# Kernel optimization log

Hardware: AMD Instinct MI355X
Metric: run time of the kernel (lower is better)

Reference implementation:

```python
import jax, jax.numpy as jnp
import numpy as np
from jax import lax

N, L, B = 256, 20, 10      # batch, max_seq (baskets), max_bas (items/basket)
D, H, ASP, K = 128, 128, 4, 16  # dim, h, aspects, nbNUM
NITEMS = 20000
H2 = 2 * H


def setup_inputs() -> dict:
    key = jax.random.key(0)
    ks = jax.random.split(key, 20)
    nrm = lambda k, shape, s=0.05: (jax.random.normal(k, shape) * s).astype(jnp.float32)
    seq = jax.random.randint(ks[0], (N, L, B), 0, NITEMS + 1)          # indices into itemEmb
    uHis = jax.random.uniform(ks[1], (N, NITEMS), dtype=jnp.float32)   # dense user history
    itemEmb = nrm(ks[2], (NITEMS + 1, D), 0.1).at[0].set(0.0)          # padding_idx=0 row zeroed
    fc1_w = nrm(ks[3], (1, L * B * D)); fc1_b = jnp.zeros((1,), jnp.float32)
    aspProju = nrm(ks[4], (ASP, 1, H))
    aspProji = nrm(ks[5], (ASP, D, H))
    dh_w = nrm(ks[6], (H, D)); dh_b = jnp.zeros((H,), jnp.float32)
    wih0 = nrm(ks[7], (4 * H2, H2)); whh0 = nrm(ks[8], (4 * H2, H2))
    bih0 = jnp.zeros((4 * H2,), jnp.float32); bhh0 = jnp.zeros((4 * H2,), jnp.float32)
    wih1 = nrm(ks[9], (4 * H2, H2)); whh1 = nrm(ks[10], (4 * H2, H2))
    bih1 = jnp.zeros((4 * H2,), jnp.float32); bhh1 = jnp.zeros((4 * H2,), jnp.float32)
    out_w = nrm(ks[11], (NITEMS, H2)); out_b = jnp.zeros((NITEMS,), jnp.float32)
    his_w = nrm(ks[12], (H2, NITEMS)); his_b = jnp.zeros((H2,), jnp.float32)
    g1_w = nrm(ks[13], (1, H2)); g1_b = jnp.zeros((1,), jnp.float32)
    g2_w = nrm(ks[14], (1, H2)); g2_b = jnp.zeros((1,), jnp.float32)
    return dict(seq=seq, uHis=uHis, itemEmb=itemEmb, fc1_w=fc1_w, fc1_b=fc1_b,
                aspProju=aspProju, aspProji=aspProji, dh_w=dh_w, dh_b=dh_b,
                wih0=wih0, whh0=whh0, bih0=bih0, bhh0=bhh0,
                wih1=wih1, whh1=whh1, bih1=bih1, bhh1=bhh1,
                out_w=out_w, out_b=out_b, his_w=his_w, his_b=his_b,
                g1_w=g1_w, g1_b=g1_b, g2_w=g2_w, g2_b=g2_b)


def _lstm_layer(x, wih, whh, bih, bhh):
    # x: [N, T, in]; PyTorch gate order i, f, g, o
    Hs = whh.shape[1]
    def step(carry, xt):
        h, c = carry
        g = xt @ wih.T + bih + h @ whh.T + bhh
        i, f, gg, o = jnp.split(g, 4, axis=-1)
        c = jax.nn.sigmoid(f) * c + jax.nn.sigmoid(i) * jnp.tanh(gg)
        h = jax.nn.sigmoid(o) * jnp.tanh(c)
        return (h, c), h
    h0 = jnp.zeros((x.shape[0], Hs), x.dtype)
    _, ys = lax.scan(step, (h0, h0), jnp.swapaxes(x, 0, 1))
    return jnp.swapaxes(ys, 0, 1)


def reference(seq, uHis, itemEmb, fc1_w, fc1_b, aspProju, aspProji, dh_w, dh_b,
              wih0, whh0, bih0, bhh0, wih1, whh1, bih1, bhh1,
              out_w, out_b, his_w, his_b, g1_w, g1_b, g2_w, g2_b):
    n, l, b = seq.shape
    embs = itemEmb[seq]                                   # [N,L,B,D]
    # MIE_user: fresh fc1 -> scalar per user, project per aspect
    u_embs = embs.reshape(n, -1) @ fc1_w.T + fc1_b        # [N,1]
    userAsp = jnp.tanh(jnp.einsum('no,aoh->nah', u_embs, aspProju))      # [N,ASP,H]
    # MIE_item
    itemAsp = jnp.tanh(jnp.einsum('nlbd,adh->nalbh', embs, aspProji))    # [N,ASP,L,B,H]
    # SNA: per-aspect exact L2 kNN over the batch (FAISS IndexFlatL2 equivalent)
    uA = jnp.transpose(jnp.tanh(userAsp), (1, 0, 2))      # [ASP,N,H] (double tanh, as in source)
    sq = jnp.sum(uA * uA, -1)                             # [ASP,N]
    dist = sq[:, :, None] + sq[:, None, :] - 2.0 * jnp.einsum('anh,amh->anm', uA, uA)
    dist = jnp.where(jnp.eye(n, dtype=bool)[None], -1.0, dist)   # self ranked first
    _, I = lax.top_k(lax.stop_gradient(-dist), K)         # [ASP,N,K] ascending distance
    I = I[:, :, 1:]                                       # drop self -> K-1 neighbors
    # sum of neighbor embeddings via multiplicity matmul (== gather+sum)
    M = jax.nn.one_hot(I, n, dtype=embs.dtype).sum(2)     # [ASP,N,N]
    nb_sum = jnp.einsum('apn,nlbd->aplbd', M, embs)       # [ASP,N,L,B,D]
    nb_h = nb_sum @ dh_w.T + dh_b                         # [ASP,N,L,B,H]
    embs_PI = jnp.transpose(nb_h.sum(axis=3), (1, 0, 2, 3))        # [N,ASP,L,H]
    embs_UI = jnp.tanh(itemAsp).sum(axis=3)               # [N,ASP,L,H] (double tanh)
    neighbAsps = jnp.concatenate([embs_UI, embs_PI], axis=-1)      # [N,ASP,L,2H]
    # raw view (not permute!) then max-pool over last dim of size ASP
    x = jnp.reshape(neighbAsps, (n, l, H2, ASP)).max(axis=-1)      # [N,L,2H]
    # 2-layer LSTM (eval mode: inter-layer dropout inactive)
    y = _lstm_layer(x, wih0, whh0, bih0, bhh0)
    y = _lstm_layer(y, wih1, whh1, bih1, bhh1)
    h_agg = jnp.tanh(y.sum(axis=1))                       # [N,2H]
    probs = jax.nn.softmax(h_agg @ out_w.T + out_b, axis=-1)       # [N,NITEMS]
    uHis_h = uHis @ his_w.T + his_b                        # [N,2H]
    gate = jax.nn.sigmoid(uHis_h @ g1_w.T + g1_b + h_agg @ g2_w.T + g2_b)  # [N,1]
    scores = gate * probs + (1.0 - gate) * uHis
    return scores
```

## Files before the change

kernel.cpp:

```cpp
#include <hip/hip_runtime.h>
#include <math.h>

#define N_ 256
#define L_ 20
#define B_ 10
#define D_ 128
#define H_ 128
#define ASP_ 4
#define KK_ 16
#define NIT_ 20000
#define H2_ 256
#define G4_ 1024
#define LBD_ 25600
#define NL_ 5120
#define NLB_ 51200

typedef __attribute__((ext_vector_type(8))) short bf16x8;
typedef __attribute__((ext_vector_type(4))) short bf16x4;
typedef __attribute__((ext_vector_type(4))) float f32x4;

__device__ __forceinline__ float sigf(float x){ return 1.0f/(1.0f+expf(-x)); }
__device__ __forceinline__ float sigf_fast(float x){
  return __builtin_amdgcn_rcpf(1.0f + __expf(-x));
}
__device__ __forceinline__ float tanh_fast(float x){
  return 1.0f - 2.0f*__builtin_amdgcn_rcpf(__expf(2.0f*x) + 1.0f);
}
__device__ __forceinline__ unsigned short f2b(float f){
  unsigned int u = __float_as_uint(f);
  unsigned int r = (u + 0x7FFFu + ((u>>16)&1u)) >> 16;
  return (unsigned short)r;
}
__device__ __forceinline__ float b2f(unsigned short b){
  return __uint_as_float(((unsigned int)b) << 16);
}

__global__ void k_gather(const int* __restrict__ seq, const float* __restrict__ itemEmb,
                         float* __restrict__ embs, unsigned short* __restrict__ ebh){
  int row = blockIdx.x;
  int t = threadIdx.x;
  int idx = seq[row];
  float v = itemEmb[idx*D_ + t];
  embs[row*D_ + t] = v;
  ebh[row*D_ + t] = f2b(v);
}

__global__ void k_fc1(const float* __restrict__ embs, const float* __restrict__ w,
                      const float* __restrict__ b, float* __restrict__ u){
  int n = blockIdx.x; int t = threadIdx.x;
  float s = 0.f;
  for (int i = t; i < LBD_; i += 256) s += embs[n*LBD_+i]*w[i];
  __shared__ float red[256];
  red[t]=s; __syncthreads();
  for (int o=128;o>0;o>>=1){ if(t<o) red[t]+=red[t+o]; __syncthreads(); }
  if(t==0) u[n]=red[0]+b[0];
}

__global__ void k_ua(const float* __restrict__ u, const float* __restrict__ proju,
                     float* __restrict__ ua){
  int i = blockIdx.x*blockDim.x + threadIdx.x;
  if(i >= ASP_*N_*H_) return;
  int h = i % H_; int n = (i/H_) % N_; int a = i/(H_*N_);
  ua[i] = tanhf(tanhf(u[n]*proju[a*H_+h]));
}

__global__ void k_sq(const float* __restrict__ ua, float* __restrict__ sq){
  int an = blockIdx.x; int t = threadIdx.x;
  float v = ua[an*H_ + t]; v *= v;
  __shared__ float red[128];
  red[t]=v; __syncthreads();
  for(int o=64;o>0;o>>=1){ if(t<o) red[t]+=red[t+o]; __syncthreads(); }
  if(t==0) sq[an]=red[0];
}

__global__ void k_dist(const float* __restrict__ ua, const float* __restrict__ sq,
                       float* __restrict__ dist){
  int n = blockIdx.x, a = blockIdx.y, m = threadIdx.x;
  __shared__ float un[H_];
  if(m < H_) un[m] = ua[(a*N_+n)*H_ + m];
  __syncthreads();
  const float* um = &ua[(a*N_+m)*H_];
  float dot=0.f;
  for(int h=0;h<H_;h++) dot += un[h]*um[h];
  float dval = sq[a*N_+n] + sq[a*N_+m] - 2.f*dot;
  if(m==n) dval = -1.0f;
  dist[(a*N_+n)*N_ + m] = dval;
}

__global__ __launch_bounds__(256) void k_topk(const float* __restrict__ dist, int* __restrict__ nbr){
  int wid = blockIdx.x*(blockDim.x>>6) + (threadIdx.x>>6);
  if(wid >= ASP_*N_) return;
  int lane = threadIdx.x & 63;
  const float* row = &dist[(long)wid*N_];
  float v[4]; int idx[4];
  #pragma unroll
  for(int j=0;j<4;j++){ int m = lane*4 + j; v[j] = row[m]; idx[j] = m; }
  for(int k=0;k<KK_;k++){
    float bv = v[0]; int bi = idx[0];
    #pragma unroll
    for(int j=1;j<4;j++)
      if(v[j] < bv || (v[j]==bv && idx[j] < bi)){ bv=v[j]; bi=idx[j]; }
    float rv = bv; int ri = bi;
    #pragma unroll
    for(int o=32;o>0;o>>=1){
      float ov = __shfl_xor(rv, o, 64);
      int   oi = __shfl_xor(ri, o, 64);
      if(ov < rv || (ov==rv && oi < ri)){ rv=ov; ri=oi; }
    }
    if((ri>>2) == lane){ v[ri&3] = 3.4e38f; idx[ri&3] = 0x7fffffff; }
    if(k>0 && lane==0) nbr[wid*(KK_-1)+(k-1)] = ri;
  }
}

__global__ void k_eb(const float* __restrict__ embs, float* __restrict__ eb){
  int nl = blockIdx.x; int d = threadIdx.x;
  float s=0.f;
  const float* p = &embs[nl*B_*D_ + d];
  for(int b=0;b<B_;b++) s += p[b*D_];
  eb[nl*D_ + d] = s;
}

__global__ void k_projb(const float* __restrict__ proji, unsigned short* __restrict__ projb){
  int i = blockIdx.x*blockDim.x + threadIdx.x;
  if(i>=ASP_*D_*H_) return;
  int h=i%H_, d=(i/H_)%D_, a=i/(D_*H_);
  projb[(a*H_ + h)*D_ + d] = f2b(proji[i]);
}

__global__ __launch_bounds__(256) void k_uimm(const unsigned short* __restrict__ ebh,
                                              const unsigned short* __restrict__ projb,
                                              float* __restrict__ na){
  __shared__ char smem[53248];
  unsigned short* As = (unsigned short*)smem;
  unsigned short* Bs = (unsigned short*)(smem + 20480);
  float*          Cs = (float*)smem;

  int mb = blockIdx.x;
  int a  = blockIdx.y;
  int tid = threadIdx.x;

  const unsigned short* asrc = ebh + (size_t)mb*10240;
  #pragma unroll
  for(int t=0;t<5;t++){
    int c = tid + t*256;
    int row = c >> 4;
    *(bf16x8*)(As + 8*(c ^ (row&7))) = *(const bf16x8*)(asrc + 8*c);
  }
  const unsigned short* bsrc = projb + a*16384;
  #pragma unroll
  for(int t=0;t<8;t++){
    int c = tid + t*256;
    int row = c >> 4;
    *(bf16x8*)(Bs + 8*(c ^ (row&7))) = *(const bf16x8*)(bsrc + 8*c);
  }
  __syncthreads();

  int lane = tid & 63, wave = tid >> 6;
  int l15 = lane & 15, l4 = lane >> 4;
  f32x4 acc[5][2] = {};
  #pragma unroll
  for(int kk=0;kk<4;kk++){
    bf16x8 bfr[2];
    #pragma unroll
    for(int tc=0;tc<2;tc++){
      int h = (wave*2+tc)*16 + l15;
      int c = h*16 + kk*4 + l4;
      bfr[tc] = *(const bf16x8*)(Bs + 8*(c ^ (h&7)));
    }
    #pragma unroll
    for(int tr=0;tr<5;tr++){
      int R = tr*16 + l15;
      int c = R*16 + kk*4 + l4;
      bf16x8 afr = *(const bf16x8*)(As + 8*(c ^ (R&7)));
      acc[tr][0] = __builtin_amdgcn_mfma_f32_16x16x32_bf16(afr, bfr[0], acc[tr][0], 0,0,0);
      acc[tr][1] = __builtin_amdgcn_mfma_f32_16x16x32_bf16(afr, bfr[1], acc[tr][1], 0,0,0);
    }
  }
  __syncthreads();

  #pragma unroll
  for(int tr=0;tr<5;tr++)
    #pragma unroll
    for(int tc=0;tc<2;tc++){
      int col = (wave*2+tc)*16 + l15;
      #pragma unroll
      for(int r=0;r<4;r++){
        int R = tr*16 + l4*4 + r;
        Cs[R*128 + col] = tanh_fast(tanh_fast(acc[tr][tc][r]));
      }
    }
  __syncthreads();

  #pragma unroll
  for(int t=0;t<4;t++){
    int oi = t*256 + tid;
    int g = oi >> 7, col = oi & 127;
    float s = 0.f;
    const float* p = Cs + g*1280 + col;
    #pragma unroll
    for(int b=0;b<10;b++) s += p[b*128];
    int nl = mb*8 + g;
    int n = nl/L_, l = nl%L_;
    na[((size_t)(n*ASP_+a)*L_ + l)*H2_ + col] = s;
  }
}

__global__ __launch_bounds__(256) void k_uhismm(const float* __restrict__ U,
    const float* __restrict__ W, const float* __restrict__ bias, float* __restrict__ C){
  __shared__ unsigned short As[2048];
  __shared__ unsigned short Bs[2048];
  int tid = threadIdx.x;
  int m0 = blockIdx.y*64, n0 = blockIdx.x*64;
  int kb0 = blockIdx.z*800;
  int row = tid & 63, q = tid >> 6;
  int lane = tid & 63, wave = tid >> 6;
  int l15 = lane & 15, l4 = lane >> 4;
  int wr = (wave>>1)*32, wc = (wave&1)*32;
  f32x4 acc[2][2] = {};
  for(int s=0;s<25;s++){
    int k0 = kb0 + s*32 + q*8;
    {
      const float* pa = &U[(size_t)(m0+row)*NIT_ + k0];
      float4 a0 = *(const float4*)pa, a1 = *(const float4*)(pa+4);
      bf16x8 av;
      av[0]=f2b(a0.x); av[1]=f2b(a0.y); av[2]=f2b(a0.z); av[3]=f2b(a0.w);
      av[4]=f2b(a1.x); av[5]=f2b(a1.y); av[6]=f2b(a1.z); av[7]=f2b(a1.w);
      *(bf16x8*)(As + 8*tid) = av;
      const float* pb = &W[(size_t)(n0+row)*NIT_ + k0];
      float4 b0 = *(const float4*)pb, b1 = *(const float4*)(pb+4);
      bf16x8 bv;
      bv[0]=f2b(b0.x); bv[1]=f2b(b0.y); bv[2]=f2b(b0.z); bv[3]=f2b(b0.w);
      bv[4]=f2b(b1.x); bv[5]=f2b(b1.y); bv[6]=f2b(b1.z); bv[7]=f2b(b1.w);
      *(bf16x8*)(Bs + 8*tid) = bv;
    }
    __syncthreads();
    bf16x8 afr[2], bfr[2];
    #pragma unroll
    for(int mt=0;mt<2;mt++) afr[mt] = *(const bf16x8*)(As + 8*(l4*64 + wr + mt*16 + l15));
    #pragma unroll
    for(int nt=0;nt<2;nt++) bfr[nt] = *(const bf16x8*)(Bs + 8*(l4*64 + wc + nt*16 + l15));
    #pragma unroll
    for(int mt=0;mt<2;mt++)
      #pragma unroll
      for(int nt=0;nt<2;nt++)
        acc[mt][nt] = __builtin_amdgcn_mfma_f32_16x16x32_bf16(afr[mt], bfr[nt], acc[mt][nt], 0,0,0);
    __syncthreads();
  }
  #pragma unroll
  for(int mt=0;mt<2;mt++)
    #pragma unroll
    for(int nt=0;nt<2;nt++){
      int col = n0 + wc + nt*16 + l15;
      #pragma unroll
      for(int r=0;r<4;r++){
        int rw = m0 + wr + mt*16 + l4*4 + r;
        float v = acc[mt][nt][r];
        if(blockIdx.z==0) v += bias[col];
        atomicAdd(&C[rw*H2_ + col], v);
      }
    }
}

__global__ __launch_bounds__(256) void k_xgmm(const float* __restrict__ A_,
    const float* __restrict__ W, const float* __restrict__ bias,
    unsigned short* __restrict__ Cb){
  __shared__ unsigned short As[2048];
  __shared__ unsigned short Bs[2048];
  int tid = threadIdx.x;
  int n0 = blockIdx.x*64, m0 = blockIdx.y*64;
  int row = tid & 63, q = tid >> 6;
  int lane = tid & 63, wave = tid >> 6;
  int l15 = lane & 15, l4 = lane >> 4;
  int wr = (wave>>1)*32, wc = (wave&1)*32;
  f32x4 acc[2][2] = {};
  for(int s=0;s<8;s++){
    int k0 = s*32 + q*8;
    {
      const float* pa = &A_[(size_t)(m0+row)*H2_ + k0];
      float4 a0 = *(const float4*)pa, a1 = *(const float4*)(pa+4);
      bf16x8 av;
      av[0]=f2b(a0.x); av[1]=f2b(a0.y); av[2]=f2b(a0.z); av[3]=f2b(a0.w);
      av[4]=f2b(a1.x); av[5]=f2b(a1.y); av[6]=f2b(a1.z); av[7]=f2b(a1.w);
      *(bf16x8*)(As + 8*tid) = av;
      const float* pb = &W[(size_t)(n0+row)*H2_ + k0];
      float4 b0 = *(const float4*)pb, b1 = *(const float4*)(pb+4);
      bf16x8 bv;
      bv[0]=f2b(b0.x); bv[1]=f2b(b0.y); bv[2]=f2b(b0.z); bv[3]=f2b(b0.w);
      bv[4]=f2b(b1.x); bv[5]=f2b(b1.y); bv[6]=f2b(b1.z); bv[7]=f2b(b1.w);
      *(bf16x8*)(Bs + 8*tid) = bv;
    }
    __syncthreads();
    bf16x8 afr[2], bfr[2];
    #pragma unroll
    for(int mt=0;mt<2;mt++) afr[mt] = *(const bf16x8*)(As + 8*(l4*64 + wr + mt*16 + l15));
    #pragma unroll
    for(int nt=0;nt<2;nt++) bfr[nt] = *(const bf16x8*)(Bs + 8*(l4*64 + wc + nt*16 + l15));
    #pragma unroll
    for(int mt=0;mt<2;mt++)
      #pragma unroll
      for(int nt=0;nt<2;nt++)
        acc[mt][nt] = __builtin_amdgcn_mfma_f32_16x16x32_bf16(afr[mt], bfr[nt], acc[mt][nt], 0,0,0);
    __syncthreads();
  }
  #pragma unroll
  for(int mt=0;mt<2;mt++)
    #pragma unroll
    for(int nt=0;nt<2;nt++){
      int col = n0 + wc + nt*16 + l15;
      float bs = bias[col];
      #pragma unroll
      for(int r=0;r<4;r++){
        int rw = m0 + wr + mt*16 + l4*4 + r;
        Cb[(size_t)rw*G4_ + col] = f2b(acc[mt][nt][r] + bs);
      }
    }
}

__global__ void k_outb(const float* __restrict__ w, unsigned short* __restrict__ wb){
  int i = blockIdx.x*blockDim.x + threadIdx.x;
  const float* p = w + (size_t)i*8;
  float4 a = *(const float4*)p, b = *(const float4*)(p+4);
  bf16x8 v;
  v[0]=f2b(a.x); v[1]=f2b(a.y); v[2]=f2b(a.z); v[3]=f2b(a.w);
  v[4]=f2b(b.x); v[5]=f2b(b.y); v[6]=f2b(b.z); v[7]=f2b(b.w);
  *(bf16x8*)(wb + (size_t)i*8) = v;
}

__global__ __launch_bounds__(256) void k_logitsmm(const unsigned short* __restrict__ Ab,
    const unsigned short* __restrict__ Wb, const float* __restrict__ bias,
    float* __restrict__ C){
  int n0 = blockIdx.x*32;
  int tid = threadIdx.x;
  int lane = tid & 63, wave = tid >> 6;
  int l15 = lane & 15, l4 = lane >> 4;
  f32x4 acc[4][2] = {};
  #pragma unroll
  for(int kk=0;kk<8;kk++){
    int k0 = kk*32 + l4*8;
    bf16x8 bfr[2];
    #pragma unroll
    for(int nt=0;nt<2;nt++)
      bfr[nt] = *(const bf16x8*)(Wb + (size_t)(n0 + nt*16 + l15)*H2_ + k0);
    #pragma unroll
    for(int mt=0;mt<4;mt++){
      bf16x8 afr = *(const bf16x8*)(Ab + (size_t)(wave*64 + mt*16 + l15)*H2_ + k0);
      acc[mt][0] = __builtin_amdgcn_mfma_f32_16x16x32_bf16(afr, bfr[0], acc[mt][0], 0,0,0);
      acc[mt][1] = __builtin_amdgcn_mfma_f32_16x16x32_bf16(afr, bfr[1], acc[mt][1], 0,0,0);
    }
  }
  #pragma unroll
  for(int mt=0;mt<4;mt++)
    #pragma unroll
    for(int nt=0;nt<2;nt++){
      int col = n0 + nt*16 + l15;
      float bs = bias[col];
      #pragma unroll
      for(int r=0;r<4;r++){
        int row = wave*64 + mt*16 + l4*4 + r;
        C[(size_t)row*NIT_ + col] = acc[mt][nt][r] + bs;
      }
    }
}

__global__ __launch_bounds__(256) void k_gemm(const float* __restrict__ A, const float* __restrict__ W,
    float* __restrict__ C, const float* __restrict__ bias,
    int M, int Nn, int K, int kchunk, int atomic_mode){
  __shared__ float As[64][17];
  __shared__ float Ws[64][17];
  int tid = threadIdx.x;
  int tx = tid & 15, ty = tid >> 4;
  int m0 = blockIdx.y*64, n0 = blockIdx.x*64;
  int kb0 = blockIdx.z*kchunk;
  int kend = kb0 + kchunk; if(kend > K) kend = K;
  float acc[4][4] = {};
  int lrow = tid >> 2;
  int lc4 = (tid & 3) * 4;
  for(int kb = kb0; kb < kend; kb += 16){
    {
      int gr = m0 + lrow;
      float4 v = make_float4(0,0,0,0);
      if(gr < M) v = *(const float4*)&A[(long)gr*K + kb + lc4];
      As[lrow][lc4+0]=v.x; As[lrow][lc4+1]=v.y; As[lrow][lc4+2]=v.z; As[lrow][lc4+3]=v.w;
      int gw = n0 + lrow;
      float4 u = make_float4(0,0,0,0);
      if(gw < Nn) u = *(const float4*)&W[(long)gw*K + kb + lc4];
      Ws[lrow][lc4+0]=u.x; Ws[lrow][lc4+1]=u.y; Ws[lrow][lc4+2]=u.z; Ws[lrow][lc4+3]=u.w;
    }
    __syncthreads();
    for(int k=0;k<16;k++){
      float av[4], wv[4];
      #pragma unroll
      for(int r=0;r<4;r++) av[r]=As[ty*4+r][k];
      #pragma unroll
      for(int c=0;c<4;c++) wv[c]=Ws[tx*4+c][k];
      #pragma unroll
      for(int r=0;r<4;r++)
        #pragma unroll
        for(int c=0;c<4;c++) acc[r][c] += av[r]*wv[c];
    }
    __syncthreads();
  }
  for(int r=0;r<4;r++){
    int row = m0 + ty*4 + r; if(row >= M) continue;
    for(int c=0;c<4;c++){
      int col = n0 + tx*4 + c; if(col >= Nn) continue;
      float v = acc[r][c];
      if(bias && blockIdx.z==0) v += bias[col];
      if(atomic_mode) atomicAdd(&C[(long)row*Nn+col], v);
      else C[(long)row*Nn+col] = v;
    }
  }
}

__global__ void k_pi(const float* __restrict__ e2, const int* __restrict__ nbr,
                     const float* __restrict__ dh_b, float* __restrict__ na){
  int n = blockIdx.x, a = blockIdx.y, h = threadIdx.x;
  __shared__ int nb[KK_-1];
  if(h < KK_-1) nb[h] = nbr[(a*N_+n)*(KK_-1)+h];
  __syncthreads();
  float bias = (float)B_ * dh_b[h];
  for(int l=0;l<L_;l++){
    float s = bias;
    for(int k=0;k<KK_-1;k++) s += e2[(long)(nb[k]*L_ + l)*H_ + h];
    na[((long)(n*ASP_+a)*L_ + l)*H2_ + H_ + h] = s;
  }
}

__global__ void k_xmax(const float* __restrict__ na, float* __restrict__ x){
  int i = blockIdx.x*blockDim.x + threadIdx.x;
  if(i >= N_*L_*H2_) return;
  int n = i / (L_*H2_);
  int j = i % (L_*H2_);
  const float* p = &na[(long)n*ASP_*L_*H2_ + 4*j];
  x[i] = fmaxf(fmaxf(p[0],p[1]), fmaxf(p[2],p[3]));
}

__global__ void k_perm(const float* __restrict__ src, float* __restrict__ dst){
  int i = blockIdx.x*blockDim.x + threadIdx.x;
  if(i >= G4_*H2_) return;
  int k = i % H2_; int j = i / H2_;
  int g = j / H2_, jj = j % H2_;
  dst[(jj*4+g)*H2_ + k] = src[i];
}
__global__ void k_permh(const float* __restrict__ src, unsigned short* __restrict__ dst){
  int i = blockIdx.x*blockDim.x + threadIdx.x;
  if(i >= G4_*H2_) return;
  int k = i % H2_; int j = i / H2_;
  int g = j / H2_, jj = j % H2_;
  dst[(jj*4+g)*H2_ + k] = f2b(src[i]);
}
__global__ void k_permb(const float* __restrict__ bih, const float* __restrict__ bhh,
                        float* __restrict__ bp){
  int j = blockIdx.x*blockDim.x + threadIdx.x;
  if(j >= G4_) return;
  int g = j / H2_, jj = j % H2_;
  bp[jj*4+g] = bih[j] + bhh[j];
}

__global__ __launch_bounds__(1024) void k_lstm_layer(
    const unsigned short* __restrict__ Whb,
    const unsigned short* __restrict__ xgb,
    float* __restrict__ Y){
  __shared__ unsigned short wc[65536];
  __shared__ unsigned short hs[2][16*H2_];
  int tid = threadIdx.x;
  int n0 = blockIdx.x * 16;
  int lane = tid & 63, wave = tid >> 6;
  int l15 = lane & 15, l4 = lane >> 4;
  int n = n0 + l15;
  float creg[4] = {0.f,0.f,0.f,0.f};
  {
    int ct0 = wave*4;
    #pragma unroll
    for(int it=0; it<8; it++){
      int c = it*64 + lane;
      int row = c >> 5;
      bf16x8 w8 = *(const bf16x8*)(Whb + (size_t)(ct0*16+row)*H2_ + (c&31)*8);
      *(bf16x8*)(wc + 8*((wave<<9) + (c ^ (row&7)))) = w8;
    }
  }
  const unsigned short* wptr[3];
  #pragma unroll
  for(int i=0;i<3;i++) wptr[i] = Whb + (size_t)((wave*4+1+i)*16 + l15)*H2_ + l4*8;
  const unsigned short* wc0 = wc + (wave<<12);
  __syncthreads();
  for(int t=0; t<L_; t++){
    bf16x4 xgv[4];
    #pragma unroll
    for(int i=0;i<4;i++){
      int jj = wave*16 + i*4 + l4;
      xgv[i] = *(const bf16x4*)(xgb + ((size_t)n*L_ + t)*G4_ + jj*4);
    }
    f32x4 acc[4] = {};
    if(t > 0){
      const unsigned short* hbuf = hs[(t+1)&1];
      bf16x8 hfr[8];
      #pragma unroll
      for(int kk=0; kk<8; kk++){
        int ch = l15*32 + kk*4 + l4;
        hfr[kk] = *(const bf16x8*)(hbuf + 8*(ch ^ (l15&7)));
      }
      #pragma unroll
      for(int kk=0; kk<8; kk++){
        bf16x8 wfr[4];
        wfr[0] = *(const bf16x8*)(wc0 + 8*((l15*32 + kk*4 + l4) ^ (l15&7)));
        #pragma unroll
        for(int i=0;i<3;i++) wfr[1+i] = *(const bf16x8*)(wptr[i] + kk*32);
        #pragma unroll
        for(int i=0;i<4;i++)
          acc[i] = __builtin_amdgcn_mfma_f32_16x16x32_bf16(wfr[i], hfr[kk], acc[i], 0,0,0);
      }
    }
    unsigned short* hout = hs[t&1];
    #pragma unroll
    for(int i=0;i<4;i++){
      int jj = wave*16 + i*4 + l4;
      float gi = acc[i][0] + b2f((unsigned short)xgv[i][0]);
      float gf = acc[i][1] + b2f((unsigned short)xgv[i][1]);
      float gg = acc[i][2] + b2f((unsigned short)xgv[i][2]);
      float go = acc[i][3] + b2f((unsigned short)xgv[i][3]);
      float cnew = sigf_fast(gf)*creg[i] + sigf_fast(gi)*tanh_fast(gg);
      creg[i] = cnew;
      float hnew = sigf_fast(go)*tanh_fast(cnew);
      Y[((size_t)n*L_ + t)*H2_ + jj] = hnew;
      int ch = l15*32 + (jj>>3);
      *(unsigned short*)((char*)hout + 16*(ch ^ (l15&7)) + (jj&7)*2) = f2b(hnew);
    }
    __syncthreads();
  }
}

__global__ void k_hagg(const float* __restrict__ y1, float* __restrict__ hagg,
                       unsigned short* __restrict__ haggb){
  int i = blockIdx.x*blockDim.x + threadIdx.x;
  if(i>=N_*H2_) return;
  int n = i / H2_, jj = i % H2_;
  float s=0.f;
  for(int t=0;t<L_;t++) s += y1[((long)n*L_+t)*H2_ + jj];
  float v = tanhf(s);
  hagg[i] = v;
  haggb[i] = f2b(v);
}

__global__ void k_gate(const float* __restrict__ uhish, const float* __restrict__ hagg,
                       const float* __restrict__ g1w, const float* __restrict__ g1b,
                       const float* __restrict__ g2w, const float* __restrict__ g2b,
                       float* __restrict__ gate){
  int n = blockIdx.x; int t = threadIdx.x;
  float s = uhish[n*H2_+t]*g1w[t] + hagg[n*H2_+t]*g2w[t];
  __shared__ float red[256];
  red[t]=s; __syncthreads();
  for(int o=128;o>0;o>>=1){ if(t<o) red[t]+=red[t+o]; __syncthreads(); }
  if(t==0) gate[n] = 1.f/(1.f+expf(-(red[0]+g1b[0]+g2b[0])));
}

__global__ void k_smstat(const float* __restrict__ logits, float* __restrict__ rowmax,
                         float* __restrict__ rowsum){
  int n = blockIdx.x; int t = threadIdx.x;
  const float* row = &logits[(long)n*NIT_];
  float m = -3.4e38f;
  for(int i=t;i<NIT_;i+=256) m = fmaxf(m, row[i]);
  __shared__ float red[256];
  __shared__ float mm;
  red[t]=m; __syncthreads();
  for(int o=128;o>0;o>>=1){ if(t<o) red[t]=fmaxf(red[t],red[t+o]); __syncthreads(); }
  if(t==0){ mm = red[0]; rowmax[n]=red[0]; }
  __syncthreads();
  float s=0.f;
  for(int i=t;i<NIT_;i+=256) s += __expf(row[i]-mm);
  __syncthreads();
  red[t]=s; __syncthreads();
  for(int o=128;o>0;o>>=1){ if(t<o) red[t]+=red[t+o]; __syncthreads(); }
  if(t==0) rowsum[n]=red[0];
}

__global__ void k_final(const float* __restrict__ logits, const float* __restrict__ rowmax,
                        const float* __restrict__ rowsum, const float* __restrict__ gate,
                        const float* __restrict__ uHis, float* __restrict__ out){
  int i = blockIdx.x*blockDim.x + threadIdx.x;
  if(i >= N_*NIT_) return;
  int n = i / NIT_;
  float g = gate[n];
  float p = __expf(logits[i]-rowmax[n]) / rowsum[n];
  out[i] = g*p + (1.f-g)*uHis[i];
}

extern "C" void kernel_launch(void* const* d_in, const int* in_sizes, int n_in,
                              void* d_out, int out_size, void* d_ws, size_t ws_size,
                              hipStream_t stream) {
  const int*   seq     = (const int*)  d_in[0];
  const float* uHis    = (const float*)d_in[1];
  const float* itemEmb = (const float*)d_in[2];
  const float* fc1_w   = (const float*)d_in[3];
  const float* fc1_b   = (const float*)d_in[4];
  const float* aspProju= (const float*)d_in[5];
  const float* aspProji= (const float*)d_in[6];
  const float* dh_w    = (const float*)d_in[7];
  const float* dh_b    = (const float*)d_in[8];
  const float* wih0    = (const float*)d_in[9];
  const float* whh0    = (const float*)d_in[10];
  const float* bih0    = (const float*)d_in[11];
  const float* bhh0    = (const float*)d_in[12];
  const float* wih1    = (const float*)d_in[13];
  const float* whh1    = (const float*)d_in[14];
  const float* bih1    = (const float*)d_in[15];
  const float* bhh1    = (const float*)d_in[16];
  const float* out_w   = (const float*)d_in[17];
  const float* out_b   = (const float*)d_in[18];
  const float* his_w   = (const float*)d_in[19];
  const float* his_b   = (const float*)d_in[20];
  const float* g1_w    = (const float*)d_in[21];
  const float* g1_b    = (const float*)d_in[22];
  const float* g2_w    = (const float*)d_in[23];
  const float* g2_b    = (const float*)d_in[24];

  float* ws = (float*)d_ws;
  float* embs = ws + 0;
  float* cub  = ws + 6553600;
  float* na   = ws + 13107200;
  float* x    = ws + 18350080;
  float* y0   = ws + 19660800;
  float* y1   = ws + 20971520;
  float* eb   = ws + 22282240;
  float* e2   = ws + 22937600;
  float* dist = ws + 23592960;
  float* ua   = ws + 23855104;
  float* projT= ws + 23986176;
  float* wp0  = ws + 24051712;
  float* whp0 = ws + 24313856;
  float* wp1  = ws + 24576000;
  float* whp1 = ws + 24838144;
  float* bp0  = ws + 25100288;
  float* bp1  = ws + 25101312;
  float* uemb = ws + 25167872;
  float* sqb  = ws + 25168128;
  int*   nbr  = (int*)(ws + 25169152);
  float* uhish= ws + 25184512;
  float* hagg = ws + 25250048;
  float* rowmax=ws + 25315584;
  float* rowsum=ws + 25315840;
  float* gateb =ws + 25316096;
  float* logits = embs;
  unsigned short* ebh   = (unsigned short*)cub;
  unsigned short* xgb   = (unsigned short*)cub;
  unsigned short* projb = (unsigned short*)projT;
  unsigned short* outwb = (unsigned short*)na;
  unsigned short* haggb = (unsigned short*)x;
  unsigned short* whb0  = (unsigned short*)whp0;
  unsigned short* whb1  = (unsigned short*)whp1;

  k_gather<<<NLB_, D_, 0, stream>>>(seq, itemEmb, embs, ebh);
  k_fc1<<<N_, 256, 0, stream>>>(embs, fc1_w, fc1_b, uemb);
  k_ua<<<(ASP_*N_*H_+255)/256, 256, 0, stream>>>(uemb, aspProju, ua);
  k_sq<<<ASP_*N_, 128, 0, stream>>>(ua, sqb);
  k_dist<<<dim3(N_,ASP_), 256, 0, stream>>>(ua, sqb, dist);
  k_topk<<<ASP_*N_/4, 256, 0, stream>>>(dist, nbr);
  k_eb<<<NL_, D_, 0, stream>>>(embs, eb);
  k_gemm<<<dim3(2, 80, 1), 256, 0, stream>>>(eb, dh_w, e2, nullptr, NL_, H_, D_, D_, 0);
  k_projb<<<(ASP_*D_*H_+255)/256, 256, 0, stream>>>(aspProji, projb);
  k_uimm<<<dim3(NL_/8, ASP_), 256, 0, stream>>>(ebh, projb, na);
  k_pi<<<dim3(N_,ASP_), H_, 0, stream>>>(e2, nbr, dh_b, na);
  k_xmax<<<(N_*L_*H2_+255)/256, 256, 0, stream>>>(na, x);
  k_outb<<<2500, 256, 0, stream>>>(out_w, outwb);
  k_perm <<<(G4_*H2_+255)/256,256,0,stream>>>(wih0, wp0);
  k_permh<<<(G4_*H2_+255)/256,256,0,stream>>>(whh0, whb0);
  k_perm <<<(G4_*H2_+255)/256,256,0,stream>>>(wih1, wp1);
  k_permh<<<(G4_*H2_+255)/256,256,0,stream>>>(whh1, whb1);
  k_permb<<<4,256,0,stream>>>(bih0,bhh0,bp0);
  k_permb<<<4,256,0,stream>>>(bih1,bhh1,bp1);
  k_xgmm<<<dim3(16,80), 256, 0, stream>>>(x, wp0, bp0, xgb);
  k_lstm_layer<<<16, 1024, 0, stream>>>(whb0, xgb, y0);
  k_xgmm<<<dim3(16,80), 256, 0, stream>>>(y0, wp1, bp1, xgb);
  k_lstm_layer<<<16, 1024, 0, stream>>>(whb1, xgb, y1);
  k_hagg<<<(N_*H2_+255)/256,256,0,stream>>>(y1, hagg, haggb);
  k_logitsmm<<<625, 256, 0, stream>>>(haggb, outwb, out_b, logits);
  hipMemsetAsync(uhish, 0, N_*H2_*sizeof(float), stream);
  k_uhismm<<<dim3(4,4,25), 256, 0, stream>>>(uHis, his_w, his_b, uhish);
  k_gate<<<N_,256,0,stream>>>(uhish, hagg, g1_w, g1_b, g2_w, g2_b, gateb);
  k_smstat<<<N_,256,0,stream>>>(logits, rowmax, rowsum);
  k_final<<<(N_*NIT_+255)/256,256,0,stream>>>(logits, rowmax, rowsum, gateb, uHis, (float*)d_out);
}
```

Before: 546.1 us.

## Split LSTM recurrence across four cooperating blocks with global h exchange

Each 16-sample group of the LSTM recurrence now runs on four 256-thread blocks instead of one 1024-thread block, so 64 CUs share the work instead of 16. Each block keeps its quarter of the recurrent weights fully in LDS, so it no longer reads three of four weight tiles from global memory every step. After each timestep the blocks publish their bf16 hidden-state slice to global memory, raise a release flag, spin on their peers' flags, and read the other slices back into shared memory. This adds a global handshake per step and relies on all four blocks of a group being resident together, or they deadlock.

```diff
diff --git a/kernel.cpp b/kernel.cpp
--- a/kernel.cpp
+++ b/kernel.cpp
@@ -457,38 +457,36 @@
   bp[jj*4+g] = bih[j] + bhh[j];
 }
 
-__global__ __launch_bounds__(1024) void k_lstm_layer(
+__global__ __launch_bounds__(256) void k_lstm_layer(
     const unsigned short* __restrict__ Whb,
     const unsigned short* __restrict__ xgb,
-    float* __restrict__ Y){
+    float* __restrict__ Y,
+    unsigned int* __restrict__ hexch,
+    int* __restrict__ flags){
   __shared__ unsigned short wc[65536];
   __shared__ unsigned short hs[2][16*H2_];
   int tid = threadIdx.x;
-  int n0 = blockIdx.x * 16;
+  int b = blockIdx.x, sg = b>>2, q = b&3;
+  int n0 = sg*16;
   int lane = tid & 63, wave = tid >> 6;
   int l15 = lane & 15, l4 = lane >> 4;
   int n = n0 + l15;
   float creg[4] = {0.f,0.f,0.f,0.f};
-  {
-    int ct0 = wave*4;
-    #pragma unroll
-    for(int it=0; it<8; it++){
-      int c = it*64 + lane;
-      int row = c >> 5;
-      bf16x8 w8 = *(const bf16x8*)(Whb + (size_t)(ct0*16+row)*H2_ + (c&31)*8);
-      *(bf16x8*)(wc + 8*((wave<<9) + (c ^ (row&7)))) = w8;
-    }
-  }
-  const unsigned short* wptr[3];
-  #pragma unroll
-  for(int i=0;i<3;i++) wptr[i] = Whb + (size_t)((wave*4+1+i)*16 + l15)*H2_ + l4*8;
-  const unsigned short* wc0 = wc + (wave<<12);
+  #pragma unroll
+  for(int it=0; it<32; it++){
+    int cidx = it*256 + tid;
+    int tl = cidx >> 9;
+    int c  = cidx & 511;
+    int row = c >> 5;
+    bf16x8 w8 = *(const bf16x8*)(Whb + (size_t)((q*16+tl)*16 + row)*H2_ + (c&31)*8);
+    *(bf16x8*)(wc + 8*((tl<<9) + (c ^ (row&7)))) = w8;
+  }
   __syncthreads();
   for(int t=0; t<L_; t++){
     bf16x4 xgv[4];
     #pragma unroll
     for(int i=0;i<4;i++){
-      int jj = wave*16 + i*4 + l4;
+      int jj = q*64 + wave*16 + i*4 + l4;
       xgv[i] = *(const bf16x4*)(xgb + ((size_t)n*L_ + t)*G4_ + jj*4);
     }
     f32x4 acc[4] = {};
@@ -503,18 +501,21 @@
       #pragma unroll
       for(int kk=0; kk<8; kk++){
         bf16x8 wfr[4];
-        wfr[0] = *(const bf16x8*)(wc0 + 8*((l15*32 + kk*4 + l4) ^ (l15&7)));
         #pragma unroll
-        for(int i=0;i<3;i++) wfr[1+i] = *(const bf16x8*)(wptr[i] + kk*32);
+        for(int i=0;i<4;i++){
+          int tl = wave*4 + i;
+          wfr[i] = *(const bf16x8*)(wc + 8*((tl<<9) + ((l15*32 + kk*4 + l4) ^ (l15&7))));
+        }
         #pragma unroll
         for(int i=0;i<4;i++)
           acc[i] = __builtin_amdgcn_mfma_f32_16x16x32_bf16(wfr[i], hfr[kk], acc[i], 0,0,0);
       }
     }
     unsigned short* hout = hs[t&1];
+    unsigned int hbits[4];
     #pragma unroll
     for(int i=0;i<4;i++){
-      int jj = wave*16 + i*4 + l4;
+      int jj = q*64 + wave*16 + i*4 + l4;
       float gi = acc[i][0] + b2f((unsigned short)xgv[i][0]);
       float gf = acc[i][1] + b2f((unsigned short)xgv[i][1]);
       float gg = acc[i][2] + b2f((unsigned short)xgv[i][2]);
@@ -523,8 +524,46 @@
       creg[i] = cnew;
       float hnew = sigf_fast(go)*tanh_fast(cnew);
       Y[((size_t)n*L_ + t)*H2_ + jj] = hnew;
+      unsigned short us = f2b(hnew);
+      hbits[i] = us;
       int ch = l15*32 + (jj>>3);
-      *(unsigned short*)((char*)hout + 16*(ch ^ (l15&7)) + (jj&7)*2) = f2b(hnew);
+      *(unsigned short*)((char*)hout + 16*(ch ^ (l15&7)) + (jj&7)*2) = us;
+    }
+    if(t < L_-1){
+      unsigned int* hx = hexch + ((size_t)(t&1)*64 + b)*512;
+      #pragma unroll
+      for(int i=0;i<4;i++){
+        unsigned int part = (unsigned int)__shfl_xor((int)hbits[i], 16, 64);
+        if((l4 & 1) == 0){
+          int jjl = wave*16 + i*4 + l4;
+          unsigned int packed = (hbits[i] & 0xFFFFu) | (part << 16);
+          __hip_atomic_store(&hx[l15*32 + (jjl>>1)], packed,
+                             __ATOMIC_RELAXED, __HIP_MEMORY_SCOPE_AGENT);
+        }
+      }
+      __syncthreads();
+      if(tid == 0)
+        __hip_atomic_store(&flags[sg*4+q], t+1, __ATOMIC_RELEASE, __HIP_MEMORY_SCOPE_AGENT);
+      if(tid < 3){
+        int qq = tid + (tid >= q ? 1 : 0);
+        while(__hip_atomic_load(&flags[sg*4+qq], __ATOMIC_ACQUIRE,
+                                __HIP_MEMORY_SCOPE_AGENT) < t+1){}
+      }
+      __syncthreads();
+      #pragma unroll
+      for(int it2=0; it2<6; it2++){
+        int idx = it2*256 + tid;
+        int qr = idx >> 9;
+        int qq = qr + (qr >= q ? 1 : 0);
+        int u  = idx & 511;
+        unsigned int pk = __hip_atomic_load(
+            &hexch[((size_t)(t&1)*64 + sg*4 + qq)*512 + u],
+            __ATOMIC_RELAXED, __HIP_MEMORY_SCOPE_AGENT);
+        int smp = u >> 5;
+        int jj  = qq*64 + (u & 31)*2;
+        int ch  = smp*32 + (jj>>3);
+        *(unsigned int*)((char*)hout + 16*(ch ^ (smp&7)) + (jj&7)*2) = pk;
+      }
     }
     __syncthreads();
   }
@@ -648,6 +687,8 @@
   unsigned short* haggb = (unsigned short*)x;
   unsigned short* whb0  = (unsigned short*)whp0;
   unsigned short* whb1  = (unsigned short*)whp1;
+  unsigned int*   hexch = (unsigned int*)dist;
+  int*            lflags= (int*)(dist + 65536);
 
   k_gather<<<NLB_, D_, 0, stream>>>(seq, itemEmb, embs, ebh);
   k_fc1<<<N_, 256, 0, stream>>>(embs, fc1_w, fc1_b, uemb);
@@ -668,10 +709,11 @@
   k_permh<<<(G4_*H2_+255)/256,256,0,stream>>>(whh1, whb1);
   k_permb<<<4,256,0,stream>>>(bih0,bhh0,bp0);
   k_permb<<<4,256,0,stream>>>(bih1,bhh1,bp1);
+  hipMemsetAsync(lflags, 0, 128*sizeof(int), stream);
   k_xgmm<<<dim3(16,80), 256, 0, stream>>>(x, wp0, bp0, xgb);
-  k_lstm_layer<<<16, 1024, 0, stream>>>(whb0, xgb, y0);
+  k_lstm_layer<<<64, 256, 0, stream>>>(whb0, xgb, y0, hexch, lflags);
   k_xgmm<<<dim3(16,80), 256, 0, stream>>>(y0, wp1, bp1, xgb);
-  k_lstm_layer<<<16, 1024, 0, stream>>>(whb1, xgb, y1);
+  k_lstm_layer<<<64, 256, 0, stream>>>(whb1, xgb, y1, hexch, lflags + 64);
   k_hagg<<<(N_*H2_+255)/256,256,0,stream>>>(y1, hagg, haggb);
   k_logitsmm<<<625, 256, 0, stream>>>(haggb, outwb, out_b, logits);
   hipMemsetAsync(uhish, 0, N_*H2_*sizeof(float), stream);
```

Result: faster. 516.3 us (-5.5%).

## Fuse small kernels: distance+topk, ua+sq, weight prep, hagg+gate, softmax+final

Applied to the files above, without the earlier changes.

Merges several small kernels into fewer launches. The distance row is kept in shared memory for the top-k step instead of going through global memory, and all weight permutations are folded into one prep kernel. hagg is fused with the gate, and softmax statistics are fused with the final blend, which cuts launch count and global round trips. The trade-off is that the softmax/output pass now runs with only 256 blocks of 512 threads, where the old elementwise final kernel had a much wider grid. Also, only one wave per block does the top-k work.

```diff
diff --git a/kernel.cpp b/kernel.cpp
--- a/kernel.cpp
+++ b/kernel.cpp
@@ -19,7 +19,6 @@
 typedef __attribute__((ext_vector_type(4))) short bf16x4;
 typedef __attribute__((ext_vector_type(4))) float f32x4;
 
-__device__ __forceinline__ float sigf(float x){ return 1.0f/(1.0f+expf(-x)); }
 __device__ __forceinline__ float sigf_fast(float x){
   return __builtin_amdgcn_rcpf(1.0f + __expf(-x));
 }
@@ -56,27 +55,24 @@
   if(t==0) u[n]=red[0]+b[0];
 }
 
-__global__ void k_ua(const float* __restrict__ u, const float* __restrict__ proju,
-                     float* __restrict__ ua){
-  int i = blockIdx.x*blockDim.x + threadIdx.x;
-  if(i >= ASP_*N_*H_) return;
-  int h = i % H_; int n = (i/H_) % N_; int a = i/(H_*N_);
-  ua[i] = tanhf(tanhf(u[n]*proju[a*H_+h]));
-}
-
-__global__ void k_sq(const float* __restrict__ ua, float* __restrict__ sq){
-  int an = blockIdx.x; int t = threadIdx.x;
-  float v = ua[an*H_ + t]; v *= v;
+__global__ void k_uasq(const float* __restrict__ u, const float* __restrict__ proju,
+                       float* __restrict__ ua, float* __restrict__ sq){
+  int an = blockIdx.x;
+  int h = threadIdx.x;
+  int a = an / N_, n = an % N_;
+  float v = tanhf(tanhf(u[n]*proju[a*H_+h]));
+  ua[an*H_ + h] = v;
   __shared__ float red[128];
-  red[t]=v; __syncthreads();
-  for(int o=64;o>0;o>>=1){ if(t<o) red[t]+=red[t+o]; __syncthreads(); }
-  if(t==0) sq[an]=red[0];
-}
-
-__global__ void k_dist(const float* __restrict__ ua, const float* __restrict__ sq,
-                       float* __restrict__ dist){
+  red[h] = v*v; __syncthreads();
+  for(int o=64;o>0;o>>=1){ if(h<o) red[h]+=red[h+o]; __syncthreads(); }
+  if(h==0) sq[an]=red[0];
+}
+
+__global__ __launch_bounds__(256) void k_disttopk(const float* __restrict__ ua,
+    const float* __restrict__ sq, int* __restrict__ nbr){
   int n = blockIdx.x, a = blockIdx.y, m = threadIdx.x;
   __shared__ float un[H_];
+  __shared__ float row[N_];
   if(m < H_) un[m] = ua[(a*N_+n)*H_ + m];
   __syncthreads();
   const float* um = &ua[(a*N_+m)*H_];
@@ -84,31 +80,29 @@
   for(int h=0;h<H_;h++) dot += un[h]*um[h];
   float dval = sq[a*N_+n] + sq[a*N_+m] - 2.f*dot;
   if(m==n) dval = -1.0f;
-  dist[(a*N_+n)*N_ + m] = dval;
-}
-
-__global__ __launch_bounds__(256) void k_topk(const float* __restrict__ dist, int* __restrict__ nbr){
-  int wid = blockIdx.x*(blockDim.x>>6) + (threadIdx.x>>6);
-  if(wid >= ASP_*N_) return;
-  int lane = threadIdx.x & 63;
-  const float* row = &dist[(long)wid*N_];
-  float v[4]; int idx[4];
-  #pragma unroll
-  for(int j=0;j<4;j++){ int m = lane*4 + j; v[j] = row[m]; idx[j] = m; }
-  for(int k=0;k<KK_;k++){
-    float bv = v[0]; int bi = idx[0];
-    #pragma unroll
-    for(int j=1;j<4;j++)
-      if(v[j] < bv || (v[j]==bv && idx[j] < bi)){ bv=v[j]; bi=idx[j]; }
-    float rv = bv; int ri = bi;
-    #pragma unroll
-    for(int o=32;o>0;o>>=1){
-      float ov = __shfl_xor(rv, o, 64);
-      int   oi = __shfl_xor(ri, o, 64);
-      if(ov < rv || (ov==rv && oi < ri)){ rv=ov; ri=oi; }
-    }
-    if((ri>>2) == lane){ v[ri&3] = 3.4e38f; idx[ri&3] = 0x7fffffff; }
-    if(k>0 && lane==0) nbr[wid*(KK_-1)+(k-1)] = ri;
+  row[m] = dval;
+  __syncthreads();
+  if(m < 64){
+    int lane = m;
+    int wid = a*N_+n;
+    float v[4]; int idx[4];
+    #pragma unroll
+    for(int j=0;j<4;j++){ int mm = lane*4 + j; v[j] = row[mm]; idx[j] = mm; }
+    for(int k=0;k<KK_;k++){
+      float bv = v[0]; int bi = idx[0];
+      #pragma unroll
+      for(int j=1;j<4;j++)
+        if(v[j] < bv || (v[j]==bv && idx[j] < bi)){ bv=v[j]; bi=idx[j]; }
+      float rv = bv; int ri = bi;
+      #pragma unroll
+      for(int o=32;o>0;o>>=1){
+        float ov = __shfl_xor(rv, o, 64);
+        int   oi = __shfl_xor(ri, o, 64);
+        if(ov < rv || (ov==rv && oi < ri)){ rv=ov; ri=oi; }
+      }
+      if((ri>>2) == lane){ v[ri&3] = 3.4e38f; idx[ri&3] = 0x7fffffff; }
+      if(k>0 && lane==0) nbr[wid*(KK_-1)+(k-1)] = ri;
+    }
   }
 }
 
@@ -120,11 +114,38 @@
   eb[nl*D_ + d] = s;
 }
 
-__global__ void k_projb(const float* __restrict__ proji, unsigned short* __restrict__ projb){
+__global__ void k_prep(const float* __restrict__ wih0, const float* __restrict__ whh0,
+                       const float* __restrict__ wih1, const float* __restrict__ whh1,
+                       const float* __restrict__ bih0, const float* __restrict__ bhh0,
+                       const float* __restrict__ bih1, const float* __restrict__ bhh1,
+                       const float* __restrict__ proji,
+                       float* __restrict__ wp0, unsigned short* __restrict__ whb0,
+                       float* __restrict__ wp1, unsigned short* __restrict__ whb1,
+                       float* __restrict__ bp0, float* __restrict__ bp1,
+                       unsigned short* __restrict__ projb){
   int i = blockIdx.x*blockDim.x + threadIdx.x;
-  if(i>=ASP_*D_*H_) return;
-  int h=i%H_, d=(i/H_)%D_, a=i/(D_*H_);
-  projb[(a*H_ + h)*D_ + d] = f2b(proji[i]);
+  if(i < 262144){
+    int k=i%H2_, j=i/H2_, g=j/H2_, jj=j%H2_;
+    wp0[(jj*4+g)*H2_+k] = wih0[i];
+  } else if(i < 524288){
+    int e=i-262144; int k=e%H2_, j=e/H2_, g=j/H2_, jj=j%H2_;
+    whb0[(jj*4+g)*H2_+k] = f2b(whh0[e]);
+  } else if(i < 786432){
+    int e=i-524288; int k=e%H2_, j=e/H2_, g=j/H2_, jj=j%H2_;
+    wp1[(jj*4+g)*H2_+k] = wih1[e];
+  } else if(i < 1048576){
+    int e=i-786432; int k=e%H2_, j=e/H2_, g=j/H2_, jj=j%H2_;
+    whb1[(jj*4+g)*H2_+k] = f2b(whh1[e]);
+  } else if(i < 1114112){
+    int e=i-1048576; int h=e%H_, d=(e/H_)%D_, aa=e/(D_*H_);
+    projb[(aa*H_+h)*D_+d] = f2b(proji[e]);
+  } else if(i < 1115136){
+    int j=i-1114112; int g=j/H2_, jj=j%H2_;
+    bp0[jj*4+g] = bih0[j] + bhh0[j];
+  } else if(i < 1116160){
+    int j=i-1115136; int g=j/H2_, jj=j%H2_;
+    bp1[jj*4+g] = bih1[j] + bhh1[j];
+  }
 }
 
 __global__ __launch_bounds__(256) void k_uimm(const unsigned short* __restrict__ ebh,
@@ -435,28 +456,6 @@
   x[i] = fmaxf(fmaxf(p[0],p[1]), fmaxf(p[2],p[3]));
 }
 
-__global__ void k_perm(const float* __restrict__ src, float* __restrict__ dst){
-  int i = blockIdx.x*blockDim.x + threadIdx.x;
-  if(i >= G4_*H2_) return;
-  int k = i % H2_; int j = i / H2_;
-  int g = j / H2_, jj = j % H2_;
-  dst[(jj*4+g)*H2_ + k] = src[i];
-}
-__global__ void k_permh(const float* __restrict__ src, unsigned short* __restrict__ dst){
-  int i = blockIdx.x*blockDim.x + threadIdx.x;
-  if(i >= G4_*H2_) return;
-  int k = i % H2_; int j = i / H2_;
-  int g = j / H2_, jj = j % H2_;
-  dst[(jj*4+g)*H2_ + k] = f2b(src[i]);
-}
-__global__ void k_permb(const float* __restrict__ bih, const float* __restrict__ bhh,
-                        float* __restrict__ bp){
-  int j = blockIdx.x*blockDim.x + threadIdx.x;
-  if(j >= G4_) return;
-  int g = j / H2_, jj = j % H2_;
-  bp[jj*4+g] = bih[j] + bhh[j];
-}
-
 __global__ __launch_bounds__(1024) void k_lstm_layer(
     const unsigned short* __restrict__ Whb,
     const unsigned short* __restrict__ xgb,
@@ -530,59 +529,50 @@
   }
 }
 
-__global__ void k_hagg(const float* __restrict__ y1, float* __restrict__ hagg,
-                       unsigned short* __restrict__ haggb){
-  int i = blockIdx.x*blockDim.x + threadIdx.x;
-  if(i>=N_*H2_) return;
-  int n = i / H2_, jj = i % H2_;
+__global__ void k_hagg_gate(const float* __restrict__ y1, const float* __restrict__ uhish,
+                            const float* __restrict__ g1w, const float* __restrict__ g1b,
+                            const float* __restrict__ g2w, const float* __restrict__ g2b,
+                            float* __restrict__ hagg, unsigned short* __restrict__ haggb,
+                            float* __restrict__ gate){
+  int n = blockIdx.x; int jj = threadIdx.x;
   float s=0.f;
   for(int t=0;t<L_;t++) s += y1[((long)n*L_+t)*H2_ + jj];
   float v = tanhf(s);
-  hagg[i] = v;
-  haggb[i] = f2b(v);
-}
-
-__global__ void k_gate(const float* __restrict__ uhish, const float* __restrict__ hagg,
-                       const float* __restrict__ g1w, const float* __restrict__ g1b,
-                       const float* __restrict__ g2w, const float* __restrict__ g2b,
-                       float* __restrict__ gate){
-  int n = blockIdx.x; int t = threadIdx.x;
-  float s = uhish[n*H2_+t]*g1w[t] + hagg[n*H2_+t]*g2w[t];
+  hagg[n*H2_+jj] = v;
+  haggb[n*H2_+jj] = f2b(v);
   __shared__ float red[256];
-  red[t]=s; __syncthreads();
-  for(int o=128;o>0;o>>=1){ if(t<o) red[t]+=red[t+o]; __syncthreads(); }
-  if(t==0) gate[n] = 1.f/(1.f+expf(-(red[0]+g1b[0]+g2b[0])));
-}
-
-__global__ void k_smstat(const float* __restrict__ logits, float* __restrict__ rowmax,
-                         float* __restrict__ rowsum){
+  red[jj] = uhish[n*H2_+jj]*g1w[jj] + v*g2w[jj];
+  __syncthreads();
+  for(int o=128;o>0;o>>=1){ if(jj<o) red[jj]+=red[jj+o]; __syncthreads(); }
+  if(jj==0) gate[n] = 1.f/(1.f+expf(-(red[0]+g1b[0]+g2b[0])));
+}
+
+__global__ __launch_bounds__(512) void k_softmax_out(const float* __restrict__ logits,
+    const float* __restrict__ gate, const float* __restrict__ uHis, float* __restrict__ out){
   int n = blockIdx.x; int t = threadIdx.x;
   const float* row = &logits[(long)n*NIT_];
   float m = -3.4e38f;
-  for(int i=t;i<NIT_;i+=256) m = fmaxf(m, row[i]);
-  __shared__ float red[256];
-  __shared__ float mm;
+  for(int i=t;i<NIT_;i+=512) m = fmaxf(m, row[i]);
+  __shared__ float red[512];
+  __shared__ float mm, ss;
   red[t]=m; __syncthreads();
-  for(int o=128;o>0;o>>=1){ if(t<o) red[t]=fmaxf(red[t],red[t+o]); __syncthreads(); }
-  if(t==0){ mm = red[0]; rowmax[n]=red[0]; }
+  for(int o=256;o>0;o>>=1){ if(t<o) red[t]=fmaxf(red[t],red[t+o]); __syncthreads(); }
+  if(t==0) mm = red[0];
   __syncthreads();
   float s=0.f;
-  for(int i=t;i<NIT_;i+=256) s += __expf(row[i]-mm);
+  for(int i=t;i<NIT_;i+=512) s += __expf(row[i]-mm);
   __syncthreads();
   red[t]=s; __syncthreads();
-  for(int o=128;o>0;o>>=1){ if(t<o) red[t]+=red[t+o]; __syncthreads(); }
-  if(t==0) rowsum[n]=red[0];
-}
-
-__global__ void k_final(const float* __restrict__ logits, const float* __restrict__ rowmax,
-                        const float* __restrict__ rowsum, const float* __restrict__ gate,
-                        const float* __restrict__ uHis, float* __restrict__ out){
-  int i = blockIdx.x*blockDim.x + threadIdx.x;
-  if(i >= N_*NIT_) return;
-  int n = i / NIT_;
+  for(int o=256;o>0;o>>=1){ if(t<o) red[t]+=red[t+o]; __syncthreads(); }
+  if(t==0) ss = red[0];
+  __syncthreads();
   float g = gate[n];
-  float p = __expf(logits[i]-rowmax[n]) / rowsum[n];
-  out[i] = g*p + (1.f-g)*uHis[i];
+  float* orow = out + (long)n*NIT_;
+  const float* urow = uHis + (long)n*NIT_;
+  for(int i=t;i<NIT_;i+=512){
+    float p = __expf(row[i]-mm)/ss;
+    orow[i] = g*p + (1.f-g)*urow[i];
+  }
 }
 
 extern "C" void kernel_launch(void* const* d_in, const int* in_sizes, int n_in,
@@ -623,7 +613,6 @@
   float* y1   = ws + 20971520;
   float* eb   = ws + 22282240;
   float* e2   = ws + 22937600;
-  float* dist = ws + 23592960;
   float* ua   = ws + 23855104;
   float* projT= ws + 23986176;
   float* wp0  = ws + 24051712;
@@ -637,8 +626,6 @@
   int*   nbr  = (int*)(ws + 25169152);
   float* uhish= ws + 25184512;
   float* hagg = ws + 25250048;
-  float* rowmax=ws + 25315584;
-  float* rowsum=ws + 25315840;
   float* gateb =ws + 25316096;
   float* logits = embs;
   unsigned short* ebh   = (unsigned short*)cub;
@@ -651,32 +638,23 @@
 
   k_gather<<<NLB_, D_, 0, stream>>>(seq, itemEmb, embs, ebh);
   k_fc1<<<N_, 256, 0, stream>>>(embs, fc1_w, fc1_b, uemb);
-  k_ua<<<(ASP_*N_*H_+255)/256, 256, 0, stream>>>(uemb, aspProju, ua);
-  k_sq<<<ASP_*N_, 128, 0, stream>>>(ua, sqb);
-  k_dist<<<dim3(N_,ASP_), 256, 0, stream>>>(ua, sqb, dist);
-  k_topk<<<ASP_*N_/4, 256, 0, stream>>>(dist, nbr);
+  k_uasq<<<ASP_*N_, 128, 0, stream>>>(uemb, aspProju, ua, sqb);
+  k_disttopk<<<dim3(N_,ASP_), 256, 0, stream>>>(ua, sqb, nbr);
   k_eb<<<NL_, D_, 0, stream>>>(embs, eb);
   k_gemm<<<dim3(2, 80, 1), 256, 0, stream>>>(eb, dh_w, e2, nullptr, NL_, H_, D_, D_, 0);
-  k_projb<<<(ASP_*D_*H_+255)/256, 256, 0, stream>>>(aspProji, projb);
+  k_prep<<<4360, 256, 0, stream>>>(wih0, whh0, wih1, whh1, bih0, bhh0, bih1, bhh1,
+                                   aspProji, wp0, whb0, wp1, whb1, bp0, bp1, projb);
   k_uimm<<<dim3(NL_/8, ASP_), 256, 0, stream>>>(ebh, projb, na);
   k_pi<<<dim3(N_,ASP_), H_, 0, stream>>>(e2, nbr, dh_b, na);
   k_xmax<<<(N_*L_*H2_+255)/256, 256, 0, stream>>>(na, x);
   k_outb<<<2500, 256, 0, stream>>>(out_w, outwb);
-  k_perm <<<(G4_*H2_+255)/256,256,0,stream>>>(wih0, wp0);
-  k_permh<<<(G4_*H2_+255)/256,256,0,stream>>>(whh0, whb0);
-  k_perm <<<(G4_*H2_+255)/256,256,0,stream>>>(wih1, wp1);
-  k_permh<<<(G4_*H2_+255)/256,256,0,stream>>>(whh1, whb1);
-  k_permb<<<4,256,0,stream>>>(bih0,bhh0,bp0);
-  k_permb<<<4,256,0,stream>>>(bih1,bhh1,bp1);
   k_xgmm<<<dim3(16,80), 256, 0, stream>>>(x, wp0, bp0, xgb);
   k_lstm_layer<<<16, 1024, 0, stream>>>(whb0, xgb, y0);
   k_xgmm<<<dim3(16,80), 256, 0, stream>>>(y0, wp1, bp1, xgb);
   k_lstm_layer<<<16, 1024, 0, stream>>>(whb1, xgb, y1);
-  k_hagg<<<(N_*H2_+255)/256,256,0,stream>>>(y1, hagg, haggb);
-  k_logitsmm<<<625, 256, 0, stream>>>(haggb, outwb, out_b, logits);
   hipMemsetAsync(uhish, 0, N_*H2_*sizeof(float), stream);
   k_uhismm<<<dim3(4,4,25), 256, 0, stream>>>(uHis, his_w, his_b, uhish);
-  k_gate<<<N_,256,0,stream>>>(uhish, hagg, g1_w, g1_b, g2_w, g2_b, gateb);
-  k_smstat<<<N_,256,0,stream>>>(logits, rowmax, rowsum);
-  k_final<<<(N_*NIT_+255)/256,256,0,stream>>>(logits, rowmax, rowsum, gateb, uHis, (float*)d_out);
-}
+  k_hagg_gate<<<N_, 256, 0, stream>>>(y1, uhish, g1_w, g1_b, g2_w, g2_b, hagg, haggb, gateb);
+  k_logitsmm<<<625, 256, 0, stream>>>(haggb, outwb, out_b, logits);
+  k_softmax_out<<<N_, 512, 0, stream>>>(logits, gateb, uHis, (float*)d_out);
+}
```

Result: faster. 522.4 us (-4.3%).
